# Optimization experiments

Measured on AMD Instinct MI355X. Metric: run time of the kernel, lower is better.

The kernel has to match this reference:

```python
import jax, jax.numpy as jnp
import numpy as np

N_HEADS = 16


def setup_inputs() -> dict:
    key = jax.random.key(0)
    k1, k2 = jax.random.split(key)
    bs, width, length = 8, 3 * N_HEADS * 64, 1024  # C=64 per head
    qkv = jax.random.normal(k1, (bs, width, length), dtype=jnp.float32)
    mask = jax.random.uniform(k2, (bs, length), dtype=jnp.float32)
    return {"qkv": qkv, "mask": mask}


def reference(qkv, mask):
    bs, width, length = qkv.shape
    ch = width // (3 * N_HEADS)
    q, k, v = jnp.split(qkv, 3, axis=1)
    # view(bs*H, ch, T): head index is inner (b*H + h ordering)
    q = q.reshape(bs * N_HEADS, ch, length)
    k = k.reshape(bs * N_HEADS, ch, length)
    v = v.reshape(bs * N_HEADS, ch, length)
    scale = 1.0 / jnp.sqrt(jnp.sqrt(jnp.asarray(ch, dtype=qkv.dtype)))
    # [bs*H, T, T] score matrix
    weight = jnp.einsum('bct,bcs->bts', q * scale, k * scale)
    # torch mask.repeat(n_heads, 1) tiles the batch dim -> jnp.tile
    m = jnp.tile(mask, (N_HEADS, 1))[:, None, :]  # [bs*H, 1, T]
    weight = weight * m
    weight = jax.nn.softmax(weight.astype(jnp.float32), axis=-1).astype(weight.dtype)
    a = jnp.einsum('bts,bcs->bct', weight, v)  # [bs*H, ch, T]
    return a.reshape(bs, N_HEADS * ch, length)
```

## Files before the change

kernel.cpp:

```cpp
#include <hip/hip_runtime.h>
#include <stdint.h>
#include <math.h>

typedef float  f32x4  __attribute__((ext_vector_type(4)));
typedef __bf16 bf16x8 __attribute__((ext_vector_type(8)));
typedef __bf16 bf16x4 __attribute__((ext_vector_type(4)));

#define MFMA16(a, b, c) __builtin_amdgcn_mfma_f32_16x16x32_bf16((a), (b), (c), 0, 0, 0)

static constexpr int kT    = 1024;
static constexpr int kLS   = 72;
static constexpr int kTile = 64 * kLS;
static constexpr size_t kTensorEl    = (size_t)128 * 16 * kTile;
static constexpr size_t kTensorBytes = kTensorEl * 2;

__device__ inline void async16(const void* g, void* l) {
  __builtin_amdgcn_global_load_lds(
      (const __attribute__((address_space(1))) void*)g,
      (__attribute__((address_space(3))) void*)l, 16, 0, 0);
}

__global__ __launch_bounds__(256, 8)
void prepass(const float* __restrict__ qkv, const float* __restrict__ mask,
             __bf16* __restrict__ qh, __bf16* __restrict__ qlo,
             __bf16* __restrict__ kh, __bf16* __restrict__ vh)
{
  __shared__ float ts[64 * 65];
  const int tid = threadIdx.x;
  const int bid = blockIdx.x, bh = bid >> 4, tile = bid & 15;
  const int b = bh >> 4, h = bh & 15, t0 = tile * 64;
  const float* __restrict__ qb = qkv + (size_t)(b * 3072 + h * 64) * kT;
  const float* __restrict__ kb = qkv + (size_t)(b * 3072 + 1024 + h * 64) * kT;
  const float* __restrict__ vb = qkv + (size_t)(b * 3072 + 2048 + h * 64) * kT;
  const float* __restrict__ mrow = mask + (size_t)(h & 7) * kT;
  const size_t tbase = ((size_t)bh * 16 + tile) * kTile;

  const int t4   = (tid & 15) * 4;
  const int crow = tid >> 4;
  const int c0   = tid & 15;
  const int rr   = tid >> 4;

  #pragma unroll
  for (int i = 0; i < 4; ++i) {
    const int c = i * 16 + crow;
    f32x4 q4 = *(const f32x4*)&qb[(size_t)c * kT + t0 + t4];
    q4 *= 0.18033688f;
    *(f32x4*)&ts[c * 65 + t4] = q4;
    f32x4 v4 = *(const f32x4*)&vb[(size_t)c * kT + t0 + t4];
    bf16x4 v4h;
    #pragma unroll
    for (int j = 0; j < 4; ++j) v4h[j] = (__bf16)v4[j];
    *(bf16x4*)&vh[tbase + c * kLS + t4] = v4h;
  }
  __syncthreads();

  #pragma unroll
  for (int i = 0; i < 4; ++i) {
    const int row = i * 16 + rr;
    bf16x4 qh4, ql4;
    #pragma unroll
    for (int j = 0; j < 4; ++j) {
      float q = ts[(c0 * 4 + j) * 65 + row];
      __bf16 qhi = (__bf16)q;
      qh4[j] = qhi; ql4[j] = (__bf16)(q - (float)qhi);
    }
    const size_t o = tbase + row * kLS + c0 * 4;
    *(bf16x4*)&qh [o] = qh4;
    *(bf16x4*)&qlo[o] = ql4;
  }
  __syncthreads();

  const f32x4 m4 = *(const f32x4*)&mrow[t0 + t4];
  #pragma unroll
  for (int i = 0; i < 4; ++i) {
    const int c = i * 16 + crow;
    f32x4 k4 = *(const f32x4*)&kb[(size_t)c * kT + t0 + t4];
    k4 *= m4;
    *(f32x4*)&ts[c * 65 + t4] = k4;
  }
  __syncthreads();

  #pragma unroll
  for (int i = 0; i < 4; ++i) {
    const int row = i * 16 + rr;
    bf16x4 kh4;
    #pragma unroll
    for (int j = 0; j < 4; ++j) kh4[j] = (__bf16)ts[(c0 * 4 + j) * 65 + row];
    *(bf16x4*)&kh[tbase + row * kLS + c0 * 4] = kh4;
  }
}

__global__ __launch_bounds__(256, 4)
void attn_main(const __bf16* __restrict__ qh, const __bf16* __restrict__ qlo,
               const __bf16* __restrict__ kh, const __bf16* __restrict__ vh,
               float* __restrict__ out)
{
  __shared__ __align__(16) __bf16 sK[2][kTile];
  __shared__ __align__(16) __bf16 sP[128 * kLS];

  const int tid  = threadIdx.x;
  const int lane = tid & 63;
  const int wave = tid >> 6;
  const int quad = lane >> 4;
  const int l15  = lane & 15;

  const int bid = blockIdx.x;
  const int bh  = bid & 127;
  const int tp  = bid >> 7;
  const int b   = bh >> 4;
  const int h   = bh & 15;
  const int t0  = tp * 128;

  const size_t hbase = (size_t)bh * 16;

  bf16x8 ones8;
  #pragma unroll
  for (int j = 0; j < 8; ++j) ones8[j] = (__bf16)1.0f;

  int ro[4];
  #pragma unroll
  for (int i = 0; i < 4; ++i) ro[i] = (i * 16 + l15) * kLS + quad * 8;

  bf16x8 qhf[2][2], qlf[2][2];
  {
    const size_t qt0 = (hbase + tp * 2 + 0) * kTile + (size_t)(wave * 16 + l15) * kLS + quad * 8;
    const size_t qt1 = qt0 + kTile;
    #pragma unroll
    for (int kc = 0; kc < 2; ++kc) {
      qhf[0][kc] = *(const bf16x8*)&qh [qt0 + kc * 32];
      qlf[0][kc] = *(const bf16x8*)&qlo[qt0 + kc * 32];
      qhf[1][kc] = *(const bf16x8*)&qh [qt1 + kc * 32];
      qlf[1][kc] = *(const bf16x8*)&qlo[qt1 + kc * 32];
    }
  }

  if (wave == 0) {
    const char* g = (const char*)(kh + hbase * kTile) + (size_t)lane * 16;
    char* l = (char*)sK[0];
    #pragma unroll
    for (int i = 0; i < 9; ++i) async16(g + i * 1024, l + i * 1024);
  }

  f32x4 O0[4], O1[4];
  #pragma unroll
  for (int cc = 0; cc < 4; ++cc) {
    O0[cc] = (f32x4){0.f, 0.f, 0.f, 0.f};
    O1[cc] = (f32x4){0.f, 0.f, 0.f, 0.f};
  }
  f32x4 L0 = (f32x4){0.f, 0.f, 0.f, 0.f};
  f32x4 L1 = (f32x4){0.f, 0.f, 0.f, 0.f};

  const int pw0 = (wave * 32 + l15) * kLS;
  const int pw1 = pw0 + 16 * kLS;

  for (int st = 0; st < 16; ++st) {
    __syncthreads();

    const __bf16* __restrict__ vb = vh + (hbase + st) * kTile;

    bf16x8 vf0[4];
    #pragma unroll
    for (int cc = 0; cc < 4; ++cc) vf0[cc] = *(const bf16x8*)&vb[ro[cc]];

    if (wave == 0 && st < 15) {
      const char* g = (const char*)(kh + (hbase + st + 1) * kTile) + (size_t)lane * 16;
      char* l = (char*)sK[(st + 1) & 1];
      #pragma unroll
      for (int i = 0; i < 9; ++i) async16(g + i * 1024, l + i * 1024);
    }

    const __bf16* __restrict__ sKc = sK[st & 1];

    #pragma unroll
    for (int sc = 0; sc < 4; ++sc) {
      bf16x8 k0 = *(const bf16x8*)&sKc[ro[sc]];
      bf16x8 k1 = *(const bf16x8*)&sKc[ro[sc] + 32];
      f32x4 a0 = (f32x4){0.f, 0.f, 0.f, 0.f};
      f32x4 a1 = (f32x4){0.f, 0.f, 0.f, 0.f};
      a0 = MFMA16(k0, qlf[0][0], a0);
      a0 = MFMA16(k0, qhf[0][0], a0);
      a0 = MFMA16(k1, qlf[0][1], a0);
      a0 = MFMA16(k1, qhf[0][1], a0);
      a1 = MFMA16(k0, qlf[1][0], a1);
      a1 = MFMA16(k0, qhf[1][0], a1);
      a1 = MFMA16(k1, qlf[1][1], a1);
      a1 = MFMA16(k1, qhf[1][1], a1);
      bf16x4 p0, p1;
      #pragma unroll
      for (int r = 0; r < 4; ++r) {
        p0[r] = (__bf16)exp2f(a0[r]);
        p1[r] = (__bf16)exp2f(a1[r]);
      }
      *(bf16x4*)&sP[pw0 + sc * 16 + quad * 4] = p0;
      *(bf16x4*)&sP[pw1 + sc * 16 + quad * 4] = p1;
    }

    bf16x8 vf1[4];
    #pragma unroll
    for (int cc = 0; cc < 4; ++cc) vf1[cc] = *(const bf16x8*)&vb[ro[cc] + 32];

    bf16x8 pb0[2], pb1[2];
    #pragma unroll
    for (int kc = 0; kc < 2; ++kc) {
      pb0[kc] = *(const bf16x8*)&sP[pw0 + kc * 32 + quad * 8];
      pb1[kc] = *(const bf16x8*)&sP[pw1 + kc * 32 + quad * 8];
    }
    L0 = MFMA16(ones8, pb0[0], L0);
    L0 = MFMA16(ones8, pb0[1], L0);
    L1 = MFMA16(ones8, pb1[0], L1);
    L1 = MFMA16(ones8, pb1[1], L1);

    #pragma unroll
    for (int cc = 0; cc < 4; ++cc) {
      O0[cc] = MFMA16(vf0[cc], pb0[0], O0[cc]);
      O0[cc] = MFMA16(vf1[cc], pb0[1], O0[cc]);
      O1[cc] = MFMA16(vf0[cc], pb1[0], O1[cc]);
      O1[cc] = MFMA16(vf1[cc], pb1[1], O1[cc]);
    }
  }

  const float inv0 = 1.0f / L0[0];
  const float inv1 = 1.0f / L1[0];
  const int tcol = t0 + wave * 16 + l15;
  float* __restrict__ obase = out + (size_t)b * (1024 * 1024) + (size_t)(h * 64) * kT;
  #pragma unroll
  for (int cc = 0; cc < 4; ++cc) {
    #pragma unroll
    for (int r = 0; r < 4; ++r) {
      const int c = cc * 16 + quad * 4 + r;
      obase[(size_t)c * kT + tcol]      = O0[cc][r] * inv0;
      obase[(size_t)c * kT + tcol + 64] = O1[cc][r] * inv1;
    }
  }
}

__global__ __launch_bounds__(256, 2)
void attn_fused(const float* __restrict__ qkv, const float* __restrict__ mask,
                float* __restrict__ out)
{
  __shared__ __align__(16) __bf16 Ahi[64 * kLS];
  __shared__ __align__(16) __bf16 Alo[64 * kLS];
  __shared__ __align__(16) __bf16 Vhi[64 * kLS];
  __shared__ __align__(16) __bf16 Vlo[64 * kLS];
  __shared__ __align__(16) __bf16 Phi[64 * kLS];
  __shared__ __align__(16) __bf16 Plo[64 * kLS];
  __shared__ __align__(16) float  ms[64];

  const int tid  = threadIdx.x;
  const int lane = tid & 63;
  const int wave = tid >> 6;
  const int quad = lane >> 4;
  const int l15  = lane & 15;

  const int bid = blockIdx.x;
  const int bh  = bid >> 4;
  const int tb  = bid & 15;
  const int b   = bh >> 4;
  const int h   = bh & 15;
  const int t0  = tb * 64;

  const float* __restrict__ qbase = qkv + (size_t)(b * 3072 + h * 64) * kT;
  const float* __restrict__ kbase = qkv + (size_t)(b * 3072 + 1024 + h * 64) * kT;
  const float* __restrict__ vbase = qkv + (size_t)(b * 3072 + 2048 + h * 64) * kT;
  const float* __restrict__ mrow  = mask + (size_t)(h & 7) * kT;

  const int sl = tid & 63;
  const int cg = tid >> 6;

  #pragma unroll
  for (int i = 0; i < 16; ++i) {
    const int c = cg * 16 + i;
    float v  = qbase[(size_t)c * kT + t0 + sl] * 0.125f;
    __bf16 hi = (__bf16)v;
    Ahi[sl * kLS + c] = hi;
    Alo[sl * kLS + c] = (__bf16)(v - (float)hi);
  }
  __syncthreads();

  bf16x8 qh[2], ql[2];
  {
    const int row = (wave * 16 + l15) * kLS;
    #pragma unroll
    for (int kc = 0; kc < 2; ++kc) {
      qh[kc] = *(const bf16x8*)&Ahi[row + kc * 32 + quad * 8];
      ql[kc] = *(const bf16x8*)&Alo[row + kc * 32 + quad * 8];
    }
  }
  __syncthreads();

  f32x4 O[4];
  #pragma unroll
  for (int cc = 0; cc < 4; ++cc) O[cc] = (f32x4){0.f, 0.f, 0.f, 0.f};
  float m_run = -__builtin_inff();
  float l_run = 0.f;

  for (int s0 = 0; s0 < kT; s0 += 64) {
    #pragma unroll
    for (int i = 0; i < 16; ++i) {
      const int c = cg * 16 + i;
      float kv   = kbase[(size_t)c * kT + s0 + sl];
      __bf16 khi = (__bf16)kv;
      Ahi[sl * kLS + c] = khi;
      Alo[sl * kLS + c] = (__bf16)(kv - (float)khi);
      float vv   = vbase[(size_t)c * kT + s0 + sl];
      __bf16 vhi = (__bf16)vv;
      Vhi[c * kLS + sl] = vhi;
      Vlo[c * kLS + sl] = (__bf16)(vv - (float)vhi);
    }
    if (tid < 64) ms[tid] = mrow[s0 + tid];
    __syncthreads();

    f32x4 S[4];
    #pragma unroll
    for (int sc = 0; sc < 4; ++sc) {
      f32x4 acc = (f32x4){0.f, 0.f, 0.f, 0.f};
      #pragma unroll
      for (int kc = 0; kc < 2; ++kc) {
        const int off = (sc * 16 + l15) * kLS + kc * 32 + quad * 8;
        bf16x8 kh8 = *(const bf16x8*)&Ahi[off];
        bf16x8 kl8 = *(const bf16x8*)&Alo[off];
        acc = MFMA16(kh8, ql[kc], acc);
        acc = MFMA16(kl8, qh[kc], acc);
        acc = MFMA16(kh8, qh[kc], acc);
      }
      S[sc] = acc;
    }

    float x[16];
    float tmax = -__builtin_inff();
    #pragma unroll
    for (int sc = 0; sc < 4; ++sc) {
      f32x4 mv = *(const f32x4*)&ms[sc * 16 + quad * 4];
      #pragma unroll
      for (int r = 0; r < 4; ++r) {
        float xv = S[sc][r] * mv[r];
        x[sc * 4 + r] = xv;
        tmax = fmaxf(tmax, xv);
      }
    }
    tmax = fmaxf(tmax, __shfl_xor(tmax, 16));
    tmax = fmaxf(tmax, __shfl_xor(tmax, 32));
    const float mnew  = fmaxf(m_run, tmax);
    const float alpha = __expf(m_run - mnew);
    float tsum = 0.f;
    #pragma unroll
    for (int i = 0; i < 16; ++i) {
      float p = __expf(x[i] - mnew);
      x[i] = p;
      tsum += p;
    }
    tsum += __shfl_xor(tsum, 16);
    tsum += __shfl_xor(tsum, 32);
    l_run = l_run * alpha + tsum;
    m_run = mnew;
    #pragma unroll
    for (int cc = 0; cc < 4; ++cc) O[cc] = O[cc] * alpha;

    const int prow = (wave * 16 + l15) * kLS;
    #pragma unroll
    for (int sc = 0; sc < 4; ++sc) {
      bf16x4 ph, pl;
      #pragma unroll
      for (int r = 0; r < 4; ++r) {
        float p   = x[sc * 4 + r];
        __bf16 hi = (__bf16)p;
        ph[r] = hi;
        pl[r] = (__bf16)(p - (float)hi);
      }
      *(bf16x4*)&Phi[prow + sc * 16 + quad * 4] = ph;
      *(bf16x4*)&Plo[prow + sc * 16 + quad * 4] = pl;
    }
    __syncthreads();

    bf16x8 pbh[2], pbl[2];
    #pragma unroll
    for (int kc = 0; kc < 2; ++kc) {
      pbh[kc] = *(const bf16x8*)&Phi[prow + kc * 32 + quad * 8];
      pbl[kc] = *(const bf16x8*)&Plo[prow + kc * 32 + quad * 8];
    }
    #pragma unroll
    for (int cc = 0; cc < 4; ++cc) {
      #pragma unroll
      for (int kc = 0; kc < 2; ++kc) {
        const int off = (cc * 16 + l15) * kLS + kc * 32 + quad * 8;
        bf16x8 v8 = *(const bf16x8*)&Vhi[off];
        bf16x8 w8 = *(const bf16x8*)&Vlo[off];
        O[cc] = MFMA16(v8, pbl[kc], O[cc]);
        O[cc] = MFMA16(w8, pbh[kc], O[cc]);
        O[cc] = MFMA16(v8, pbh[kc], O[cc]);
      }
    }
    __syncthreads();
  }

  const float inv  = 1.0f / l_run;
  const int   tcol = t0 + wave * 16 + l15;
  float* __restrict__ obase = out + (size_t)b * (1024 * 1024) + (size_t)(h * 64) * kT;
  #pragma unroll
  for (int cc = 0; cc < 4; ++cc) {
    #pragma unroll
    for (int r = 0; r < 4; ++r) {
      const int c = cc * 16 + quad * 4 + r;
      obase[(size_t)c * kT + tcol] = O[cc][r] * inv;
    }
  }
}

extern "C" void kernel_launch(void* const* d_in, const int* in_sizes, int n_in,
                              void* d_out, int out_size, void* d_ws, size_t ws_size,
                              hipStream_t stream)
{
  const float* qkv  = (const float*)d_in[0];
  const float* mask = (const float*)d_in[1];
  float* out = (float*)d_out;
  (void)in_sizes; (void)n_in; (void)out_size;

  if (ws_size >= 4 * kTensorBytes) {
    char* w = (char*)d_ws;
    __bf16* qh  = (__bf16*)(w + 0 * kTensorBytes);
    __bf16* qlo = (__bf16*)(w + 1 * kTensorBytes);
    __bf16* kh  = (__bf16*)(w + 2 * kTensorBytes);
    __bf16* vh  = (__bf16*)(w + 3 * kTensorBytes);
    prepass<<<dim3(2048), dim3(256), 0, stream>>>(qkv, mask, qh, qlo, kh, vh);
    attn_main<<<dim3(1024), dim3(256), 0, stream>>>(qh, qlo, kh, vh, out);
  } else {
    attn_fused<<<dim3(2048), dim3(256), 0, stream>>>(qkv, mask, out);
  }
}
```

Measured before the change: 241.9 us.

## Fuse Q split-bf16 conversion into attention kernel and spread K prefetch across waves

```diff
diff --git a/kernel.cpp b/kernel.cpp
--- a/kernel.cpp
+++ b/kernel.cpp
@@ -7,6 +7,7 @@
 typedef __bf16 bf16x4 __attribute__((ext_vector_type(4)));
 
 #define MFMA16(a, b, c) __builtin_amdgcn_mfma_f32_16x16x32_bf16((a), (b), (c), 0, 0, 0)
+#define EXP2(x) __builtin_amdgcn_exp2f(x)
 
 static constexpr int kT    = 1024;
 static constexpr int kLS   = 72;
@@ -22,14 +23,12 @@
 
 __global__ __launch_bounds__(256, 8)
 void prepass(const float* __restrict__ qkv, const float* __restrict__ mask,
-             __bf16* __restrict__ qh, __bf16* __restrict__ qlo,
              __bf16* __restrict__ kh, __bf16* __restrict__ vh)
 {
   __shared__ float ts[64 * 65];
   const int tid = threadIdx.x;
   const int bid = blockIdx.x, bh = bid >> 4, tile = bid & 15;
   const int b = bh >> 4, h = bh & 15, t0 = tile * 64;
-  const float* __restrict__ qb = qkv + (size_t)(b * 3072 + h * 64) * kT;
   const float* __restrict__ kb = qkv + (size_t)(b * 3072 + 1024 + h * 64) * kT;
   const float* __restrict__ vb = qkv + (size_t)(b * 3072 + 2048 + h * 64) * kT;
   const float* __restrict__ mrow = mask + (size_t)(h & 7) * kT;
@@ -37,49 +36,24 @@
 
   const int t4   = (tid & 15) * 4;
   const int crow = tid >> 4;
-  const int c0   = tid & 15;
-  const int rr   = tid >> 4;
-
-  #pragma unroll
-  for (int i = 0; i < 4; ++i) {
-    const int c = i * 16 + crow;
-    f32x4 q4 = *(const f32x4*)&qb[(size_t)c * kT + t0 + t4];
-    q4 *= 0.18033688f;
-    *(f32x4*)&ts[c * 65 + t4] = q4;
-    f32x4 v4 = *(const f32x4*)&vb[(size_t)c * kT + t0 + t4];
-    bf16x4 v4h;
-    #pragma unroll
-    for (int j = 0; j < 4; ++j) v4h[j] = (__bf16)v4[j];
-    *(bf16x4*)&vh[tbase + c * kLS + t4] = v4h;
-  }
-  __syncthreads();
-
-  #pragma unroll
-  for (int i = 0; i < 4; ++i) {
-    const int row = i * 16 + rr;
-    bf16x4 qh4, ql4;
-    #pragma unroll
-    for (int j = 0; j < 4; ++j) {
-      float q = ts[(c0 * 4 + j) * 65 + row];
-      __bf16 qhi = (__bf16)q;
-      qh4[j] = qhi; ql4[j] = (__bf16)(q - (float)qhi);
-    }
-    const size_t o = tbase + row * kLS + c0 * 4;
-    *(bf16x4*)&qh [o] = qh4;
-    *(bf16x4*)&qlo[o] = ql4;
-  }
-  __syncthreads();
-
   const f32x4 m4 = *(const f32x4*)&mrow[t0 + t4];
+
   #pragma unroll
   for (int i = 0; i < 4; ++i) {
     const int c = i * 16 + crow;
     f32x4 k4 = *(const f32x4*)&kb[(size_t)c * kT + t0 + t4];
     k4 *= m4;
     *(f32x4*)&ts[c * 65 + t4] = k4;
+    f32x4 v4 = *(const f32x4*)&vb[(size_t)c * kT + t0 + t4];
+    bf16x4 v4h;
+    #pragma unroll
+    for (int j = 0; j < 4; ++j) v4h[j] = (__bf16)v4[j];
+    *(bf16x4*)&vh[tbase + c * kLS + t4] = v4h;
   }
   __syncthreads();
 
+  const int c0 = tid & 15;
+  const int rr = tid >> 4;
   #pragma unroll
   for (int i = 0; i < 4; ++i) {
     const int row = i * 16 + rr;
@@ -91,7 +65,7 @@
 }
 
 __global__ __launch_bounds__(256, 4)
-void attn_main(const __bf16* __restrict__ qh, const __bf16* __restrict__ qlo,
+void attn_main(const float* __restrict__ qkv,
                const __bf16* __restrict__ kh, const __bf16* __restrict__ vh,
                float* __restrict__ out)
 {
@@ -123,22 +97,43 @@
 
   bf16x8 qhf[2][2], qlf[2][2];
   {
-    const size_t qt0 = (hbase + tp * 2 + 0) * kTile + (size_t)(wave * 16 + l15) * kLS + quad * 8;
-    const size_t qt1 = qt0 + kTile;
-    #pragma unroll
-    for (int kc = 0; kc < 2; ++kc) {
-      qhf[0][kc] = *(const bf16x8*)&qh [qt0 + kc * 32];
-      qlf[0][kc] = *(const bf16x8*)&qlo[qt0 + kc * 32];
-      qhf[1][kc] = *(const bf16x8*)&qh [qt1 + kc * 32];
-      qlf[1][kc] = *(const bf16x8*)&qlo[qt1 + kc * 32];
-    }
-  }
-
-  if (wave == 0) {
+    float* ts = (float*)sK;
+    const float* __restrict__ qb = qkv + (size_t)(b * 3072 + h * 64) * kT;
+    const int t4   = (tid & 15) * 4;
+    const int crow = tid >> 4;
+    const int trow = wave * 16 + l15;
+    #pragma unroll
+    for (int half = 0; half < 2; ++half) {
+      const int tq0 = t0 + half * 64;
+      #pragma unroll
+      for (int i = 0; i < 4; ++i) {
+        const int c = i * 16 + crow;
+        f32x4 q4 = *(const f32x4*)&qb[(size_t)c * kT + tq0 + t4];
+        q4 *= 0.18033688f;
+        *(f32x4*)&ts[c * 65 + t4] = q4;
+      }
+      __syncthreads();
+      #pragma unroll
+      for (int kc = 0; kc < 2; ++kc) {
+        bf16x8 hf, lf;
+        #pragma unroll
+        for (int j = 0; j < 8; ++j) {
+          float q = ts[(kc * 32 + quad * 8 + j) * 65 + trow];
+          __bf16 hi = (__bf16)q;
+          hf[j] = hi;
+          lf[j] = (__bf16)(q - (float)hi);
+        }
+        qhf[half][kc] = hf;
+        qlf[half][kc] = lf;
+      }
+      __syncthreads();
+    }
+  }
+
+  {
     const char* g = (const char*)(kh + hbase * kTile) + (size_t)lane * 16;
     char* l = (char*)sK[0];
-    #pragma unroll
-    for (int i = 0; i < 9; ++i) async16(g + i * 1024, l + i * 1024);
+    for (int i = wave; i < 9; i += 4) async16(g + i * 1024, l + i * 1024);
   }
 
   f32x4 O0[4], O1[4];
@@ -162,11 +157,10 @@
     #pragma unroll
     for (int cc = 0; cc < 4; ++cc) vf0[cc] = *(const bf16x8*)&vb[ro[cc]];
 
-    if (wave == 0 && st < 15) {
+    if (st < 15) {
       const char* g = (const char*)(kh + (hbase + st + 1) * kTile) + (size_t)lane * 16;
       char* l = (char*)sK[(st + 1) & 1];
-      #pragma unroll
-      for (int i = 0; i < 9; ++i) async16(g + i * 1024, l + i * 1024);
+      for (int i = wave; i < 9; i += 4) async16(g + i * 1024, l + i * 1024);
     }
 
     const __bf16* __restrict__ sKc = sK[st & 1];
@@ -188,8 +182,8 @@
       bf16x4 p0, p1;
       #pragma unroll
       for (int r = 0; r < 4; ++r) {
-        p0[r] = (__bf16)exp2f(a0[r]);
-        p1[r] = (__bf16)exp2f(a1[r]);
+        p0[r] = (__bf16)EXP2(a0[r]);
+        p1[r] = (__bf16)EXP2(a1[r]);
       }
       *(bf16x4*)&sP[pw0 + sc * 16 + quad * 4] = p0;
       *(bf16x4*)&sP[pw1 + sc * 16 + quad * 4] = p1;
@@ -415,14 +409,12 @@
   float* out = (float*)d_out;
   (void)in_sizes; (void)n_in; (void)out_size;
 
-  if (ws_size >= 4 * kTensorBytes) {
+  if (ws_size >= 2 * kTensorBytes) {
     char* w = (char*)d_ws;
-    __bf16* qh  = (__bf16*)(w + 0 * kTensorBytes);
-    __bf16* qlo = (__bf16*)(w + 1 * kTensorBytes);
-    __bf16* kh  = (__bf16*)(w + 2 * kTensorBytes);
-    __bf16* vh  = (__bf16*)(w + 3 * kTensorBytes);
-    prepass<<<dim3(2048), dim3(256), 0, stream>>>(qkv, mask, qh, qlo, kh, vh);
-    attn_main<<<dim3(1024), dim3(256), 0, stream>>>(qh, qlo, kh, vh, out);
+    __bf16* kh = (__bf16*)(w + 0 * kTensorBytes);
+    __bf16* vh = (__bf16*)(w + 1 * kTensorBytes);
+    prepass<<<dim3(2048), dim3(256), 0, stream>>>(qkv, mask, kh, vh);
+    attn_main<<<dim3(1024), dim3(256), 0, stream>>>(qkv, kh, vh, out);
   } else {
     attn_fused<<<dim3(2048), dim3(256), 0, stream>>>(qkv, mask, out);
   }
```

New measurement: 210.2 us. 13.1% less time.
